# Performance work log

Measured on AMD Instinct MI355X. Metric: run time of the kernel, lower is better.

Reference implementation:

```python
import jax, jax.numpy as jnp
import numpy as np

N = 40000          # spots (nodes)
G = 3000           # genes (input features)
C = 20             # num_classes
E = N * 16         # edges (avg degree 16)


def _uniform(key, shape, stdv):
    return jax.random.uniform(key, shape, jnp.float32, -stdv, stdv)


def _linear_params(key, n_in, n_out):
    # torch Linear default init: U(-1/sqrt(in), 1/sqrt(in)); stored as [in, out]
    k1, k2 = jax.random.split(key)
    s = 1.0 / np.sqrt(n_in)
    return _uniform(k1, (n_in, n_out), s), _uniform(k2, (n_out,), s)


def setup_inputs() -> dict:
    key = jax.random.key(0)
    ks = jax.random.split(key, 32)
    x = jax.random.normal(ks[0], (N, G), jnp.float32)
    adj_rows = jax.random.randint(ks[1], (E,), 0, N, jnp.int32)
    adj_cols = jax.random.randint(ks[2], (E,), 0, N, jnp.int32)
    adj_vals = jax.random.uniform(ks[3], (E,), jnp.float32)

    # GCN weights: GraphConvolution init U(-1/sqrt(out), 1/sqrt(out)), no bias
    def gcn_w(k, fi, fo):
        return _uniform(k, (fi, fo), 1.0 / np.sqrt(fo))

    inp = {
        "x": x, "adj_rows": adj_rows, "adj_cols": adj_cols, "adj_vals": adj_vals,
        "W1": gcn_w(ks[4], G, 512), "W2": gcn_w(ks[5], 512, 256),
        "W3": gcn_w(ks[6], 256, 128), "W4": gcn_w(ks[7], 128, 128),
        "W5": gcn_w(ks[8], 128, C),
    }
    # AE linear layers
    for name, (fi, fo), k in [
        ("enc1", (G, 512), ks[9]), ("enc2", (512, 256), ks[10]),
        ("enc3", (256, 128), ks[11]), ("zl", (128, 128), ks[12]),
        ("dec1", (128, 128), ks[13]), ("dec2", (128, 256), ks[14]),
        ("dec3", (256, 512), ks[15]), ("xbar", (512, G), ks[16]),
    ]:
        w, b = _linear_params(k, fi, fo)
        inp[name + "_w"], inp[name + "_b"] = w, b
    # Attention projection vectors (Linear(in_size, 1, bias=False))
    inp["a1"] = _uniform(ks[17], (512,), 1.0 / np.sqrt(512))
    inp["a2"] = _uniform(ks[18], (256,), 1.0 / np.sqrt(256))
    inp["a3"] = _uniform(ks[19], (128,), 1.0 / np.sqrt(128))
    inp["a4"] = _uniform(ks[20], (128,), 1.0 / np.sqrt(128))
    inp["scale"] = jax.random.normal(ks[21], (G,), jnp.float32)
    inp["additive"] = jax.random.normal(ks[22], (G,), jnp.float32)
    return inp


def _spmm(rows, cols, vals, dense, n):
    # out[r] = sum_e vals[e] * dense[cols[e]] for rows[e]==r  (sparse [n,n] @ dense)
    return jax.ops.segment_sum(vals[:, None] * dense[cols], rows, num_segments=n)


def _gcn(x, rows, cols, vals, W, n, active=True):
    out = _spmm(rows, cols, vals, x @ W, n)
    return jax.nn.relu(out) if active else out


def _attn(h, t, a):
    # stack two [N,D] branches, softmax over the branch axis, weighted sum
    z = jnp.stack([h, t], axis=1)           # [N,2,D]
    w = jnp.einsum('nbd,d->nb', z, a)        # [N,2]
    beta = jax.nn.softmax(w, axis=1)
    return jnp.einsum('nb,nbd->nd', beta, z)


def reference(x, adj_rows, adj_cols, adj_vals,
              W1, W2, W3, W4, W5,
              enc1_w, enc1_b, enc2_w, enc2_b, enc3_w, enc3_b, zl_w, zl_b,
              dec1_w, dec1_b, dec2_w, dec2_b, dec3_w, dec3_b, xbar_w, xbar_b,
              a1, a2, a3, a4, scale, additive):
    n = x.shape[0]
    # autoencoder
    t1 = jax.nn.relu(x @ enc1_w + enc1_b)
    t2 = jax.nn.relu(t1 @ enc2_w + enc2_b)
    t3 = jax.nn.relu(t2 @ enc3_w + enc3_b)
    z = t3 @ zl_w + zl_b
    d1 = jax.nn.relu(z @ dec1_w + dec1_b)
    d2 = jax.nn.relu(d1 @ dec2_w + dec2_b)
    d3 = jax.nn.relu(d2 @ dec3_w + dec3_b)
    x_bar = d3 @ xbar_w + xbar_b
    # GCN stack with attention-fused AE skip connections
    h = _gcn(x, adj_rows, adj_cols, adj_vals, W1, n)
    emb = _attn(h, t1, a1)
    h = _gcn(emb, adj_rows, adj_cols, adj_vals, W2, n)
    emb = _attn(h, t2, a2)
    h = _gcn(emb, adj_rows, adj_cols, adj_vals, W3, n)
    emb = _attn(h, t3, a3)
    h = _gcn(emb, adj_rows, adj_cols, adj_vals, W4, n)
    emb = _attn(h, z, a4)
    output = _gcn(emb, adj_rows, adj_cols, adj_vals, W5, n, active=False)
    return output, x_bar, jax.nn.sigmoid(scale), jnp.exp(additive)
```

## Files before the change

kernel.cpp:

```cpp
#include <hip/hip_runtime.h>
#include <cmath>

typedef unsigned short u16;
typedef unsigned int u32;
typedef __attribute__((ext_vector_type(8))) short short8;
typedef __attribute__((ext_vector_type(4))) short short4v;
typedef __attribute__((ext_vector_type(4))) float f32x4;

__device__ __forceinline__ float bf2f(u16 h) {
  union { u32 u; float f; } v; v.u = ((u32)h) << 16; return v.f;
}
__device__ __forceinline__ u16 f2bf(float f) {
  union { float f; u32 u; } v; v.f = f;
  u32 u = v.u;
  u32 r = (u + 0x7FFFu + ((u >> 16) & 1u)) >> 16;
  return (u16)r;
}

__global__ void convx_kernel(const float* __restrict__ x, u16* __restrict__ A0) {
  int idx = blockIdx.x * 256 + threadIdx.x;
  int r = blockIdx.y;
  if (idx >= 752) return;
  short4v o;
  if (r < 40000 && idx < 750) {
    float4 v = *(const float4*)(x + (size_t)r * 3000 + idx * 4);
    o[0] = (short)f2bf(v.x); o[1] = (short)f2bf(v.y);
    o[2] = (short)f2bf(v.z); o[3] = (short)f2bf(v.w);
  } else {
    o[0] = 0; o[1] = 0; o[2] = 0; o[3] = 0;
  }
  *(short4v*)(A0 + (size_t)r * 3008 + idx * 4) = o;
}

__global__ void convw_kernel(const float* __restrict__ W, u16* __restrict__ Wt,
                             int K, int N, int Kp) {
  int k = blockIdx.x * 256 + threadIdx.x;
  int n = blockIdx.y;
  if (k >= Kp) return;
  float v = (k < K && n < N) ? W[(size_t)k * N + n] : 0.f;
  Wt[(size_t)n * Kp + k] = f2bf(v);
}

__global__ void zero_kernel(int* p, int n) {
  int i = blockIdx.x * 256 + threadIdx.x;
  if (i < n) p[i] = 0;
}
__global__ void count_kernel(const int* __restrict__ rows, int* __restrict__ counts, int E) {
  int i = blockIdx.x * 256 + threadIdx.x;
  if (i < E) atomicAdd(&counts[rows[i]], 1);
}
__global__ __launch_bounds__(1024) void scan_kernel(const int* __restrict__ counts,
                                                    int* __restrict__ rowptr,
                                                    int* __restrict__ cursor, int n) {
  __shared__ int buf[1024];
  __shared__ int carry_s;
  int tid = threadIdx.x;
  if (tid == 0) carry_s = 0;
  __syncthreads();
  for (int base = 0; base < n; base += 1024) {
    int i = base + tid;
    int v = (i < n) ? counts[i] : 0;
    buf[tid] = v;
    __syncthreads();
    for (int off = 1; off < 1024; off <<= 1) {
      int tv = (tid >= off) ? buf[tid - off] : 0;
      __syncthreads();
      buf[tid] += tv;
      __syncthreads();
    }
    int incl = buf[tid];
    int carry = carry_s;
    if (i < n) { int ex = carry + incl - v; rowptr[i] = ex; cursor[i] = ex; }
    __syncthreads();
    if (tid == 1023) carry_s = carry + incl;
    __syncthreads();
  }
  if (tid == 0) rowptr[n] = carry_s;
}
__global__ void scatter_kernel(const int* __restrict__ rows, const int* __restrict__ cols,
                               const float* __restrict__ vals, int* __restrict__ cursor,
                               int* __restrict__ cols_s, float* __restrict__ vals_s, int E) {
  int i = blockIdx.x * 256 + threadIdx.x;
  if (i < E) {
    int r = rows[i];
    int p = atomicAdd(&cursor[r], 1);
    cols_s[p] = cols[i];
    vals_s[p] = vals[i];
  }
}

#define BM 128
#define BN 128
#define BK 32

template <bool BIAS, bool RELU, bool OUTBF16, int CH>
__global__ __launch_bounds__(256, 2) void gemm_bf16(
    const u16* __restrict__ A, int lda, const u16* __restrict__ Bt, int ldb,
    void* __restrict__ C1, int ldc,
    const float* __restrict__ bias, int M, int Nreal, int K, int MT, int NT) {
  __shared__ __align__(16) u16 As[2][BM * BK];
  __shared__ __align__(16) u16 Bs[2][BN * BK];
  const int lin = blockIdx.x;
  const int per = CH * NT;
  const int g = lin / per;
  const int r0 = lin - g * per;
  const int bx0 = g * CH;
  const int cw = min(CH, MT - bx0);
  const int bx = bx0 + r0 % cw;
  const int by = r0 / cw;

  const int tid = threadIdx.x;
  const int lane = tid & 63;
  const int wave = tid >> 6;
  const int mblk = bx * BM;
  const int nblk = by * BN;
  const int wm = (wave & 1) * 64;
  const int wn = (wave >> 1) * 64;
  const int ml = lane & 15;
  const int kg = lane >> 4;

  f32x4 acc[4][4];
#pragma unroll
  for (int i = 0; i < 4; ++i)
#pragma unroll
    for (int j = 0; j < 4; ++j) acc[i][j] = (f32x4)(0.f);

  const int nk = K / BK;
  const int sr = tid >> 2;
  const int sc = (tid & 3) * 8;
  const u16* gA0 = A + (size_t)(mblk + sr) * lda + sc;
  const u16* gA1 = A + (size_t)(mblk + sr + 64) * lda + sc;
  const u16* gB0 = Bt + (size_t)(nblk + sr) * ldb + sc;
  const u16* gB1 = Bt + (size_t)(nblk + sr + 64) * ldb + sc;

  auto stage = [&](int buf, int kt) {
    const int ko = kt * BK;
    u16* lA = &As[buf][0] + wave * 512;
    u16* lB = &Bs[buf][0] + wave * 512;
    __builtin_amdgcn_global_load_lds((const void*)(gA0 + ko), (void*)lA, 16, 0, 0);
    __builtin_amdgcn_global_load_lds((const void*)(gA1 + ko), (void*)(lA + 2048), 16, 0, 0);
    __builtin_amdgcn_global_load_lds((const void*)(gB0 + ko), (void*)lB, 16, 0, 0);
    __builtin_amdgcn_global_load_lds((const void*)(gB1 + ko), (void*)(lB + 2048), 16, 0, 0);
  };

  stage(0, 0);
  asm volatile("s_waitcnt vmcnt(0)" ::: "memory");
  __syncthreads();

  int cur = 0;
  for (int kt = 0; kt < nk; ++kt) {
    if (kt + 1 < nk) stage(cur ^ 1, kt + 1);
    short8 af[4], bfr[4];
#pragma unroll
    for (int i = 0; i < 4; ++i) {
      af[i] = *(const short8*)&As[cur][(wm + i * 16 + ml) * BK + kg * 8];
      bfr[i] = *(const short8*)&Bs[cur][(wn + i * 16 + ml) * BK + kg * 8];
    }
#pragma unroll
    for (int i = 0; i < 4; ++i)
#pragma unroll
      for (int j = 0; j < 4; ++j)
        acc[i][j] = __builtin_amdgcn_mfma_f32_16x16x32_bf16(af[i], bfr[j], acc[i][j], 0, 0, 0);
    asm volatile("s_waitcnt vmcnt(0)" ::: "memory");
    __syncthreads();
    cur ^= 1;
  }

#pragma unroll
  for (int i = 0; i < 4; ++i) {
    const int row0 = mblk + wm + i * 16 + kg * 4;
#pragma unroll
    for (int j = 0; j < 4; ++j) {
      const int col = nblk + wn + j * 16 + ml;
      if (col < Nreal) {
        float bv = BIAS ? bias[col] : 0.f;
#pragma unroll
        for (int r = 0; r < 4; ++r) {
          const int row = row0 + r;
          if (row < M) {
            float v = acc[i][j][r] + bv;
            if (RELU) v = fmaxf(v, 0.f);
            if (OUTBF16)
              ((u16*)C1)[(size_t)row * ldc + col] = f2bf(v);
            else
              ((float*)C1)[(size_t)row * ldc + col] = v;
          }
        }
      }
    }
  }
}

template <int MODE>
__global__ __launch_bounds__(512, 1) void gemm256(
    const u16* __restrict__ A, int lda, const u16* __restrict__ Bt, int ldb,
    void* __restrict__ C1, void* __restrict__ C2, int ldc,
    const float* __restrict__ bias, int M, int Nreal, int K, int NT) {
  __shared__ __align__(16) u16 lds[2][2][256 * 64];
  const int tid = threadIdx.x;
  const int lane = tid & 63;
  const int wave = tid >> 6;
  const int wm = wave >> 2;
  const int wn = wave & 3;
  const int ml = lane & 15;
  const int kg = lane >> 4;

  const int bx = blockIdx.x / NT;
  const int by = blockIdx.x % NT;
  const int mblk = bx * 256;
  const int nblk = by * 256;

  f32x4 acc[8][4];
#pragma unroll
  for (int i = 0; i < 8; ++i)
#pragma unroll
    for (int j = 0; j < 4; ++j) acc[i][j] = (f32x4)(0.f);

  const int srow = tid >> 3;
  const int clog = (tid & 7) ^ (srow & 7);
  const size_t abase = (size_t)(mblk + srow) * lda + clog * 8;
  const size_t bbase = (size_t)(nblk + srow) * ldb + clog * 8;
  const int NKT = K / 64;

  auto stageA = [&](int d, int kt, int h) {
    u16* dst = &lds[d][0][0] + h * 4096 + wave * 512;
    const u16* src = A + abase + (size_t)h * 64 * lda + kt * 64;
    __builtin_amdgcn_global_load_lds((const void*)src, (void*)dst, 16, 0, 0);
  };
  auto stageB = [&](int d, int kt, int h) {
    u16* dst = &lds[d][1][0] + h * 4096 + wave * 512;
    const u16* src = Bt + bbase + (size_t)h * 64 * ldb + kt * 64;
    __builtin_amdgcn_global_load_lds((const void*)src, (void*)dst, 16, 0, 0);
  };
  auto stagePair = [&](int d, int kt, int q) {
    if (q == 0)      { stageB(d, kt, 0); stageB(d, kt, 1); }
    else if (q == 1) { stageB(d, kt, 2); stageB(d, kt, 3); }
    else if (q == 2) { stageA(d, kt, 0); stageA(d, kt, 2); }
    else             { stageA(d, kt, 1); stageA(d, kt, 3); }
  };
  auto readA = [&](int d, int im, int kk) -> short8 {
    const int r = wm * 128 + im * 16 + ml;
    const int ch = (kk * 4 + kg) ^ (r & 7);
    return *(const short8*)&lds[d][0][r * 64 + ch * 8];
  };
  auto readB = [&](int d, int j, int kk) -> short8 {
    const int r = wn * 64 + j * 16 + ml;
    const int ch = (kk * 4 + kg) ^ (r & 7);
    return *(const short8*)&lds[d][1][r * 64 + ch * 8];
  };

#pragma unroll
  for (int q = 0; q < 4; ++q) stagePair(0, 0, q);
  asm volatile("s_waitcnt vmcnt(2)" ::: "memory");
  __builtin_amdgcn_s_barrier();

  for (int kt = 0; kt < NKT; ++kt) {
    const int d = kt & 1;
    const bool more = (kt + 1 < NKT);
    short8 bf2[4][2];
#pragma unroll
    for (int q = 0; q < 4; ++q) {
      if (q == 0) {
#pragma unroll
        for (int j = 0; j < 4; ++j) { bf2[j][0] = readB(d, j, 0); bf2[j][1] = readB(d, j, 1); }
      }
      short8 a00 = readA(d, 2 * q, 0);
      short8 a01 = readA(d, 2 * q, 1);
      short8 a10 = readA(d, 2 * q + 1, 0);
      short8 a11 = readA(d, 2 * q + 1, 1);
      if (more) stagePair(d ^ 1, kt + 1, q);
      __builtin_amdgcn_s_barrier();
      asm volatile("s_waitcnt lgkmcnt(0)" ::: "memory");
      __builtin_amdgcn_s_setprio(1);
#pragma unroll
      for (int j = 0; j < 4; ++j) {
        acc[2 * q][j]     = __builtin_amdgcn_mfma_f32_16x16x32_bf16(a00, bf2[j][0], acc[2 * q][j], 0, 0, 0);
        acc[2 * q + 1][j] = __builtin_amdgcn_mfma_f32_16x16x32_bf16(a10, bf2[j][0], acc[2 * q + 1][j], 0, 0, 0);
      }
#pragma unroll
      for (int j = 0; j < 4; ++j) {
        acc[2 * q][j]     = __builtin_amdgcn_mfma_f32_16x16x32_bf16(a01, bf2[j][1], acc[2 * q][j], 0, 0, 0);
        acc[2 * q + 1][j] = __builtin_amdgcn_mfma_f32_16x16x32_bf16(a11, bf2[j][1], acc[2 * q + 1][j], 0, 0, 0);
      }
      __builtin_amdgcn_s_setprio(0);
      if (q == 1) {
        if (more) asm volatile("s_waitcnt vmcnt(4)" ::: "memory");
        else      asm volatile("s_waitcnt vmcnt(0)" ::: "memory");
      }
      if (q == 3 && more) asm volatile("s_waitcnt vmcnt(2)" ::: "memory");
      __builtin_amdgcn_s_barrier();
    }
  }

  const int crow0 = mblk + wm * 128;
  const int ccol0 = nblk + wn * 64;
  if (MODE == 0) {
    const bool second = (nblk >= 512);
#pragma unroll
    for (int i = 0; i < 8; ++i) {
      const int row0 = crow0 + i * 16 + kg * 4;
#pragma unroll
      for (int j = 0; j < 4; ++j) {
        const int col = ccol0 + j * 16 + ml;
        const float bv = second ? 0.f : bias[col];
#pragma unroll
        for (int r = 0; r < 4; ++r) {
          const int row = row0 + r;
          if (row < M) {
            float v = acc[i][j][r] + bv;
            if (!second) v = fmaxf(v, 0.f);
            u16* dst = second ? (u16*)C2 : (u16*)C1;
            dst[(size_t)row * 512 + (second ? col - 512 : col)] = f2bf(v);
          }
        }
      }
    }
  } else {
#pragma unroll
    for (int i = 0; i < 8; ++i) {
      const int row0 = crow0 + i * 16 + kg * 4;
#pragma unroll
      for (int j = 0; j < 4; ++j) {
        const int col = ccol0 + j * 16 + ml;
        if (col < Nreal) {
          const float bv = bias[col];
#pragma unroll
          for (int r = 0; r < 4; ++r) {
            const int row = row0 + r;
            if (row < M)
              ((float*)C1)[(size_t)row * ldc + col] = acc[i][j][r] + bv;
          }
        }
      }
    }
  }
}

template <int D, bool RELU>
__global__ __launch_bounds__(256) void spmm_vec(const int* __restrict__ rowptr,
                                                const int* __restrict__ colidx,
                                                const float* __restrict__ vals,
                                                const u16* __restrict__ X,
                                                u16* __restrict__ Y) {
  constexpr int VE = D / 64;
  const int wave = threadIdx.x >> 6, lane = threadIdx.x & 63;
  const int row = blockIdx.x * 4 + wave;
  const int co = lane * VE;
  float acc[VE];
#pragma unroll
  for (int j = 0; j < VE; ++j) acc[j] = 0.f;
  const int s = rowptr[row], e = rowptr[row + 1];
  for (int i = s; i < e; ++i) {
    const int c = colidx[i];
    const float v = vals[i];
    const u16* xr = X + (size_t)c * D + co;
    if constexpr (VE == 8) {
      short8 x8 = *(const short8*)xr;
#pragma unroll
      for (int j = 0; j < 8; ++j) acc[j] += v * bf2f((u16)x8[j]);
    } else if constexpr (VE == 4) {
      short4v x4 = *(const short4v*)xr;
#pragma unroll
      for (int j = 0; j < 4; ++j) acc[j] += v * bf2f((u16)x4[j]);
    } else {
      u32 x2 = *(const u32*)xr;
      acc[0] += v * bf2f((u16)(x2 & 0xffffu));
      acc[1] += v * bf2f((u16)(x2 >> 16));
    }
  }
  u16* yr = Y + (size_t)row * D + co;
  if constexpr (VE == 8) {
    short8 o;
#pragma unroll
    for (int j = 0; j < 8; ++j) { float f = RELU ? fmaxf(acc[j], 0.f) : acc[j]; o[j] = (short)f2bf(f); }
    *(short8*)yr = o;
  } else if constexpr (VE == 4) {
    short4v o;
#pragma unroll
    for (int j = 0; j < 4; ++j) { float f = RELU ? fmaxf(acc[j], 0.f) : acc[j]; o[j] = (short)f2bf(f); }
    *(short4v*)yr = o;
  } else {
    float f0 = RELU ? fmaxf(acc[0], 0.f) : acc[0];
    float f1 = RELU ? fmaxf(acc[1], 0.f) : acc[1];
    *(u32*)yr = (u32)f2bf(f0) | ((u32)f2bf(f1) << 16);
  }
}

__global__ __launch_bounds__(64) void spmm_out_kernel(const int* __restrict__ rowptr,
                                                      const int* __restrict__ colidx,
                                                      const float* __restrict__ vals,
                                                      const u16* __restrict__ X,
                                                      float* __restrict__ Y) {
  int row = blockIdx.x;
  int c = threadIdx.x;
  float acc = 0.f;
  int s = rowptr[row], e = rowptr[row + 1];
  for (int i = s; i < e; ++i) {
    int col = colidx[i];
    float v = vals[i];
    if (c < 20) acc += v * bf2f(X[(size_t)col * 20 + c]);
  }
  if (c < 20) Y[(size_t)row * 20 + c] = acc;
}

template <int D>
__global__ __launch_bounds__(256) void attn_vec(const u16* __restrict__ h,
                                                const u16* __restrict__ t,
                                                const float* __restrict__ a,
                                                u16* __restrict__ emb) {
  constexpr int VE = D / 64;
  const int wave = threadIdx.x >> 6, lane = threadIdx.x & 63;
  const int row = blockIdx.x * 4 + wave;
  const int co = lane * VE;
  const u16* hr = h + (size_t)row * D + co;
  const u16* tr = t + (size_t)row * D + co;
  float hv[VE], tv[VE];
  if constexpr (VE == 8) {
    short8 h8 = *(const short8*)hr, t8 = *(const short8*)tr;
#pragma unroll
    for (int j = 0; j < 8; ++j) { hv[j] = bf2f((u16)h8[j]); tv[j] = bf2f((u16)t8[j]); }
  } else if constexpr (VE == 4) {
    short4v h4 = *(const short4v*)hr, t4 = *(const short4v*)tr;
#pragma unroll
    for (int j = 0; j < 4; ++j) { hv[j] = bf2f((u16)h4[j]); tv[j] = bf2f((u16)t4[j]); }
  } else {
    u32 h2 = *(const u32*)hr, t2 = *(const u32*)tr;
    hv[0] = bf2f((u16)(h2 & 0xffffu)); hv[1] = bf2f((u16)(h2 >> 16));
    tv[0] = bf2f((u16)(t2 & 0xffffu)); tv[1] = bf2f((u16)(t2 >> 16));
  }
  float wh = 0.f, wt = 0.f;
#pragma unroll
  for (int j = 0; j < VE; ++j) {
    float av = a[co + j];
    wh += av * hv[j];
    wt += av * tv[j];
  }
  for (int off = 32; off; off >>= 1) {
    wh += __shfl_xor(wh, off);
    wt += __shfl_xor(wt, off);
  }
  float m = fmaxf(wh, wt);
  float e1 = expf(wh - m), e2 = expf(wt - m);
  float inv = 1.f / (e1 + e2);
  float b1 = e1 * inv, b2 = e2 * inv;
  u16* er = emb + (size_t)row * D + co;
  if constexpr (VE == 8) {
    short8 o;
#pragma unroll
    for (int j = 0; j < 8; ++j) o[j] = (short)f2bf(b1 * hv[j] + b2 * tv[j]);
    *(short8*)er = o;
  } else if constexpr (VE == 4) {
    short4v o;
#pragma unroll
    for (int j = 0; j < 4; ++j) o[j] = (short)f2bf(b1 * hv[j] + b2 * tv[j]);
    *(short4v*)er = o;
  } else {
    *(u32*)er = (u32)f2bf(b1 * hv[0] + b2 * tv[0]) | ((u32)f2bf(b1 * hv[1] + b2 * tv[1]) << 16);
  }
}

__global__ __launch_bounds__(64) void xw5_kernel(const u16* __restrict__ emb,
                                                 const float* __restrict__ W5,
                                                 u16* __restrict__ xw5) {
  int row = blockIdx.x;
  int c = threadIdx.x;
  if (c >= 20) return;
  const short8* er = (const short8*)(emb + (size_t)row * 128);
  float acc = 0.f;
#pragma unroll
  for (int k8 = 0; k8 < 16; ++k8) {
    short8 v = er[k8];
#pragma unroll
    for (int j = 0; j < 8; ++j) acc += bf2f((u16)v[j]) * W5[(k8 * 8 + j) * 20 + c];
  }
  xw5[(size_t)row * 20 + c] = f2bf(acc);
}

__global__ void sig_exp_kernel(const float* __restrict__ scale, const float* __restrict__ additive,
                               float* __restrict__ osig, float* __restrict__ oexp, int g) {
  int i = blockIdx.x * 256 + threadIdx.x;
  if (i < g) {
    osig[i] = 1.f / (1.f + expf(-scale[i]));
    oexp[i] = expf(additive[i]);
  }
}

extern "C" void kernel_launch(void* const* d_in, const int* in_sizes, int n_in,
                              void* d_out, int out_size, void* d_ws, size_t ws_size,
                              hipStream_t stream) {
  (void)n_in; (void)out_size; (void)ws_size;
  const float* x      = (const float*)d_in[0];
  const int*   arows  = (const int*)d_in[1];
  const int*   acols  = (const int*)d_in[2];
  const float* avals  = (const float*)d_in[3];
  const float* W1     = (const float*)d_in[4];
  const float* W2     = (const float*)d_in[5];
  const float* W3     = (const float*)d_in[6];
  const float* W4     = (const float*)d_in[7];
  const float* W5     = (const float*)d_in[8];
  const float* enc1_w = (const float*)d_in[9],  *enc1_b = (const float*)d_in[10];
  const float* enc2_w = (const float*)d_in[11], *enc2_b = (const float*)d_in[12];
  const float* enc3_w = (const float*)d_in[13], *enc3_b = (const float*)d_in[14];
  const float* zl_w   = (const float*)d_in[15], *zl_b   = (const float*)d_in[16];
  const float* dec1_w = (const float*)d_in[17], *dec1_b = (const float*)d_in[18];
  const float* dec2_w = (const float*)d_in[19], *dec2_b = (const float*)d_in[20];
  const float* dec3_w = (const float*)d_in[21], *dec3_b = (const float*)d_in[22];
  const float* xbar_w = (const float*)d_in[23], *xbar_b = (const float*)d_in[24];
  const float* a1 = (const float*)d_in[25], *a2 = (const float*)d_in[26];
  const float* a3 = (const float*)d_in[27], *a4 = (const float*)d_in[28];
  const float* scale = (const float*)d_in[29], *additive = (const float*)d_in[30];

  const int E = in_sizes[1];
  const int N = 40000, G = 3000, Kx = 3008;
  const int Mp = 40192;

  float* out      = (float*)d_out;
  float* out_gcn  = out;
  float* out_xbar = out + (size_t)N * 20;
  float* out_sig  = out_xbar + (size_t)N * G;
  float* out_exp  = out_sig + G;

  char* wsb = (char*)d_ws;
  size_t off = 0;
  auto alloc = [&](size_t b) -> void* {
    void* p = wsb + off;
    off = (off + b + 255) & ~(size_t)255;
    return p;
  };
  u16* A0    = (u16*)alloc((size_t)Mp * Kx * 2);
  u16* t1    = (u16*)alloc((size_t)Mp * 512 * 2);
  u16* t2    = (u16*)alloc((size_t)Mp * 256 * 2);
  u16* t3    = (u16*)alloc((size_t)Mp * 128 * 2);
  u16* zb    = (u16*)alloc((size_t)Mp * 128 * 2);
  u16* dd1   = (u16*)alloc((size_t)Mp * 128 * 2);
  u16* dd2   = (u16*)alloc((size_t)Mp * 256 * 2);
  u16* dd3   = (u16*)alloc((size_t)Mp * 512 * 2);
  u16* xw    = (u16*)alloc((size_t)Mp * 512 * 2);
  u16* hb    = (u16*)alloc((size_t)Mp * 512 * 2);
  u16* emb   = (u16*)alloc((size_t)Mp * 512 * 2);
  u16* xw5   = (u16*)alloc((size_t)N * 20 * 2);
  u16* catT  = (u16*)alloc((size_t)1024 * Kx * 2);
  u16* enc2T = (u16*)alloc((size_t)256 * 512 * 2);
  u16* enc3T = (u16*)alloc((size_t)128 * 256 * 2);
  u16* zlT   = (u16*)alloc((size_t)128 * 128 * 2);
  u16* dec1T = (u16*)alloc((size_t)128 * 128 * 2);
  u16* dec2T = (u16*)alloc((size_t)256 * 128 * 2);
  u16* dec3T = (u16*)alloc((size_t)512 * 256 * 2);
  u16* xbarT = (u16*)alloc((size_t)3072 * 512 * 2);
  u16* W2T   = (u16*)alloc((size_t)256 * 512 * 2);
  u16* W3T   = (u16*)alloc((size_t)128 * 256 * 2);
  u16* W4T   = (u16*)alloc((size_t)128 * 128 * 2);
  int* counts = (int*)alloc((size_t)N * 4);
  int* rowptr = (int*)alloc((size_t)(N + 1) * 4);
  int* cursor = (int*)alloc((size_t)N * 4);
  int* colss  = (int*)alloc((size_t)E * 4);
  float* valss = (float*)alloc((size_t)E * 4);

  convx_kernel<<<dim3(3, Mp), 256, 0, stream>>>(x, A0);
  auto convw = [&](const float* W, u16* Wt, int K, int Nw, int Kp, int Np) {
    convw_kernel<<<dim3((Kp + 255) / 256, Np), 256, 0, stream>>>(W, Wt, K, Nw, Kp);
  };
  convw(enc1_w, catT,             3000, 512, Kx, 512);
  convw(W1,     catT + 512 * Kx,  3000, 512, Kx, 512);
  convw(enc2_w, enc2T, 512, 256, 512, 256);
  convw(enc3_w, enc3T, 256, 128, 256, 128);
  convw(zl_w,   zlT,   128, 128, 128, 128);
  convw(dec1_w, dec1T, 128, 128, 128, 128);
  convw(dec2_w, dec2T, 128, 256, 128, 256);
  convw(dec3_w, dec3T, 256, 512, 256, 512);
  convw(xbar_w, xbarT, 512, 3000, 512, 3072);
  convw(W2,     W2T,   512, 256, 512, 256);
  convw(W3,     W3T,   256, 128, 256, 128);
  convw(W4,     W4T,   128, 128, 128, 128);

  zero_kernel<<<(N + 255) / 256, 256, 0, stream>>>(counts, N);
  count_kernel<<<(E + 255) / 256, 256, 0, stream>>>(arows, counts, E);
  scan_kernel<<<1, 1024, 0, stream>>>(counts, rowptr, cursor, N);
  scatter_kernel<<<(E + 255) / 256, 256, 0, stream>>>(arows, acols, avals, cursor, colss, valss, E);

  const int MT = 313;
  const int MT2 = 157;
  gemm256<0><<<MT2 * 4, 512, 0, stream>>>(A0, Kx, catT, Kx, t1, xw, 512, enc1_b, N, 1024, Kx, 4);
  gemm_bf16<true, true, true, 32><<<MT * 2, 256, 0, stream>>>(
      t1, 512, enc2T, 512, t2, 256, enc2_b, N, 256, 512, MT, 2);
  gemm_bf16<true, true, true, 32><<<MT * 1, 256, 0, stream>>>(
      t2, 256, enc3T, 256, t3, 128, enc3_b, N, 128, 256, MT, 1);
  gemm_bf16<true, false, true, 32><<<MT * 1, 256, 0, stream>>>(
      t3, 128, zlT, 128, zb, 128, zl_b, N, 128, 128, MT, 1);
  gemm_bf16<true, true, true, 32><<<MT * 1, 256, 0, stream>>>(
      zb, 128, dec1T, 128, dd1, 128, dec1_b, N, 128, 128, MT, 1);
  gemm_bf16<true, true, true, 32><<<MT * 2, 256, 0, stream>>>(
      dd1, 128, dec2T, 128, dd2, 256, dec2_b, N, 256, 128, MT, 2);
  gemm_bf16<true, true, true, 32><<<MT * 4, 256, 0, stream>>>(
      dd2, 256, dec3T, 256, dd3, 512, dec3_b, N, 512, 256, MT, 4);
  gemm256<1><<<MT2 * 12, 512, 0, stream>>>(dd3, 512, xbarT, 512, out_xbar, nullptr, 3000, xbar_b, N, 3000, 512, 12);

  spmm_vec<512, true><<<N / 4, 256, 0, stream>>>(rowptr, colss, valss, xw, hb);
  attn_vec<512><<<N / 4, 256, 0, stream>>>(hb, t1, a1, emb);
  gemm_bf16<false, false, true, 32><<<MT * 2, 256, 0, stream>>>(
      emb, 512, W2T, 512, xw, 256, nullptr, N, 256, 512, MT, 2);
  spmm_vec<256, true><<<N / 4, 256, 0, stream>>>(rowptr, colss, valss, xw, hb);
  attn_vec<256><<<N / 4, 256, 0, stream>>>(hb, t2, a2, emb);
  gemm_bf16<false, false, true, 32><<<MT * 1, 256, 0, stream>>>(
      emb, 256, W3T, 256, xw, 128, nullptr, N, 128, 256, MT, 1);
  spmm_vec<128, true><<<N / 4, 256, 0, stream>>>(rowptr, colss, valss, xw, hb);
  attn_vec<128><<<N / 4, 256, 0, stream>>>(hb, t3, a3, emb);
  gemm_bf16<false, false, true, 32><<<MT * 1, 256, 0, stream>>>(
      emb, 128, W4T, 128, xw, 128, nullptr, N, 128, 128, MT, 1);
  spmm_vec<128, true><<<N / 4, 256, 0, stream>>>(rowptr, colss, valss, xw, hb);
  attn_vec<128><<<N / 4, 256, 0, stream>>>(hb, zb, a4, emb);

  xw5_kernel<<<N, 64, 0, stream>>>(emb, W5, xw5);
  spmm_out_kernel<<<N, 64, 0, stream>>>(rowptr, colss, valss, xw5, out_gcn);

  sig_exp_kernel<<<(G + 255) / 256, 256, 0, stream>>>(scale, additive, out_sig, out_exp, G);
}
```

Measured before the change: 1.484 ms.

## Group-swizzle gemm256 tiles, stage full next K-tile upfront, reuse for dec3

After: 1.514 ms. Within noise of the previous version (+2.0%).

```diff
diff --git a/kernel.cpp b/kernel.cpp
--- a/kernel.cpp
+++ b/kernel.cpp
@@ -191,11 +191,11 @@
   }
 }
 
-template <int MODE>
+template <bool BIAS, bool RELU, bool OUTBF16, bool SPLIT>
 __global__ __launch_bounds__(512, 1) void gemm256(
     const u16* __restrict__ A, int lda, const u16* __restrict__ Bt, int ldb,
     void* __restrict__ C1, void* __restrict__ C2, int ldc,
-    const float* __restrict__ bias, int M, int Nreal, int K, int NT) {
+    const float* __restrict__ bias, int M, int Nreal, int K, int MT2, int NT) {
   __shared__ __align__(16) u16 lds[2][2][256 * 64];
   const int tid = threadIdx.x;
   const int lane = tid & 63;
@@ -205,8 +205,11 @@
   const int ml = lane & 15;
   const int kg = lane >> 4;
 
-  const int bx = blockIdx.x / NT;
-  const int by = blockIdx.x % NT;
+  const int grp = blockIdx.x / (8 * NT);
+  const int rr = blockIdx.x % (8 * NT);
+  const int nb = min(8, MT2 - grp * 8);
+  const int bx = grp * 8 + rr % nb;
+  const int by = rr / nb;
   const int mblk = bx * 256;
   const int nblk = by * 256;
 
@@ -232,11 +235,9 @@
     const u16* src = Bt + bbase + (size_t)h * 64 * ldb + kt * 64;
     __builtin_amdgcn_global_load_lds((const void*)src, (void*)dst, 16, 0, 0);
   };
-  auto stagePair = [&](int d, int kt, int q) {
-    if (q == 0)      { stageB(d, kt, 0); stageB(d, kt, 1); }
-    else if (q == 1) { stageB(d, kt, 2); stageB(d, kt, 3); }
-    else if (q == 2) { stageA(d, kt, 0); stageA(d, kt, 2); }
-    else             { stageA(d, kt, 1); stageA(d, kt, 3); }
+  auto stageAll = [&](int d, int kt) {
+    stageB(d, kt, 0); stageB(d, kt, 1); stageB(d, kt, 2); stageB(d, kt, 3);
+    stageA(d, kt, 0); stageA(d, kt, 2); stageA(d, kt, 1); stageA(d, kt, 3);
   };
   auto readA = [&](int d, int im, int kk) -> short8 {
     const int r = wm * 128 + im * 16 + ml;
@@ -249,8 +250,7 @@
     return *(const short8*)&lds[d][1][r * 64 + ch * 8];
   };
 
-#pragma unroll
-  for (int q = 0; q < 4; ++q) stagePair(0, 0, q);
+  stageAll(0, 0);
   asm volatile("s_waitcnt vmcnt(2)" ::: "memory");
   __builtin_amdgcn_s_barrier();
 
@@ -261,6 +261,7 @@
 #pragma unroll
     for (int q = 0; q < 4; ++q) {
       if (q == 0) {
+        if (more) stageAll(d ^ 1, kt + 1);
 #pragma unroll
         for (int j = 0; j < 4; ++j) { bf2[j][0] = readB(d, j, 0); bf2[j][1] = readB(d, j, 1); }
       }
@@ -268,7 +269,6 @@
       short8 a01 = readA(d, 2 * q, 1);
       short8 a10 = readA(d, 2 * q + 1, 0);
       short8 a11 = readA(d, 2 * q + 1, 1);
-      if (more) stagePair(d ^ 1, kt + 1, q);
       __builtin_amdgcn_s_barrier();
       asm volatile("s_waitcnt lgkmcnt(0)" ::: "memory");
       __builtin_amdgcn_s_setprio(1);
@@ -283,8 +283,8 @@
         acc[2 * q + 1][j] = __builtin_amdgcn_mfma_f32_16x16x32_bf16(a11, bf2[j][1], acc[2 * q + 1][j], 0, 0, 0);
       }
       __builtin_amdgcn_s_setprio(0);
-      if (q == 1) {
-        if (more) asm volatile("s_waitcnt vmcnt(4)" ::: "memory");
+      if (q == 0) {
+        if (more) asm volatile("s_waitcnt vmcnt(8)" ::: "memory");
         else      asm volatile("s_waitcnt vmcnt(0)" ::: "memory");
       }
       if (q == 3 && more) asm volatile("s_waitcnt vmcnt(2)" ::: "memory");
@@ -294,14 +294,14 @@
 
   const int crow0 = mblk + wm * 128;
   const int ccol0 = nblk + wn * 64;
-  if (MODE == 0) {
-    const bool second = (nblk >= 512);
-#pragma unroll
-    for (int i = 0; i < 8; ++i) {
-      const int row0 = crow0 + i * 16 + kg * 4;
-#pragma unroll
-      for (int j = 0; j < 4; ++j) {
-        const int col = ccol0 + j * 16 + ml;
+#pragma unroll
+  for (int i = 0; i < 8; ++i) {
+    const int row0 = crow0 + i * 16 + kg * 4;
+#pragma unroll
+    for (int j = 0; j < 4; ++j) {
+      const int col = ccol0 + j * 16 + ml;
+      if (SPLIT) {
+        const bool second = (nblk >= 512);
         const float bv = second ? 0.f : bias[col];
 #pragma unroll
         for (int r = 0; r < 4; ++r) {
@@ -313,22 +313,18 @@
             dst[(size_t)row * 512 + (second ? col - 512 : col)] = f2bf(v);
           }
         }
-      }
-    }
-  } else {
-#pragma unroll
-    for (int i = 0; i < 8; ++i) {
-      const int row0 = crow0 + i * 16 + kg * 4;
-#pragma unroll
-      for (int j = 0; j < 4; ++j) {
-        const int col = ccol0 + j * 16 + ml;
-        if (col < Nreal) {
-          const float bv = bias[col];
-#pragma unroll
-          for (int r = 0; r < 4; ++r) {
-            const int row = row0 + r;
-            if (row < M)
-              ((float*)C1)[(size_t)row * ldc + col] = acc[i][j][r] + bv;
+      } else if (col < Nreal) {
+        const float bv = BIAS ? bias[col] : 0.f;
+#pragma unroll
+        for (int r = 0; r < 4; ++r) {
+          const int row = row0 + r;
+          if (row < M) {
+            float v = acc[i][j][r] + bv;
+            if (RELU) v = fmaxf(v, 0.f);
+            if (OUTBF16)
+              ((u16*)C1)[(size_t)row * ldc + col] = f2bf(v);
+            else
+              ((float*)C1)[(size_t)row * ldc + col] = v;
           }
         }
       }
@@ -580,7 +576,8 @@
 
   const int MT = 313;
   const int MT2 = 157;
-  gemm256<0><<<MT2 * 4, 512, 0, stream>>>(A0, Kx, catT, Kx, t1, xw, 512, enc1_b, N, 1024, Kx, 4);
+  gemm256<false, false, true, true><<<MT2 * 4, 512, 0, stream>>>(
+      A0, Kx, catT, Kx, t1, xw, 512, enc1_b, N, 1024, Kx, MT2, 4);
   gemm_bf16<true, true, true, 32><<<MT * 2, 256, 0, stream>>>(
       t1, 512, enc2T, 512, t2, 256, enc2_b, N, 256, 512, MT, 2);
   gemm_bf16<true, true, true, 32><<<MT * 1, 256, 0, stream>>>(
@@ -591,9 +588,10 @@
       zb, 128, dec1T, 128, dd1, 128, dec1_b, N, 128, 128, MT, 1);
   gemm_bf16<true, true, true, 32><<<MT * 2, 256, 0, stream>>>(
       dd1, 128, dec2T, 128, dd2, 256, dec2_b, N, 256, 128, MT, 2);
-  gemm_bf16<true, true, true, 32><<<MT * 4, 256, 0, stream>>>(
-      dd2, 256, dec3T, 256, dd3, 512, dec3_b, N, 512, 256, MT, 4);
-  gemm256<1><<<MT2 * 12, 512, 0, stream>>>(dd3, 512, xbarT, 512, out_xbar, nullptr, 3000, xbar_b, N, 3000, 512, 12);
+  gemm256<true, true, true, false><<<MT2 * 2, 512, 0, stream>>>(
+      dd2, 256, dec3T, 256, dd3, nullptr, 512, dec3_b, N, 512, 256, MT2, 2);
+  gemm256<true, false, false, false><<<MT2 * 12, 512, 0, stream>>>(
+      dd3, 512, xbarT, 512, out_xbar, nullptr, 3000, xbar_b, N, 3000, 512, MT2, 12);
 
   spmm_vec<512, true><<<N / 4, 256, 0, stream>>>(rowptr, colss, valss, xw, hb);
   attn_vec<512><<<N / 4, 256, 0, stream>>>(hb, t1, a1, emb);
```
